# Kernel optimization log

Measured on AMD Instinct MI355X. Metric: run time of the kernel, lower is better.

Reference implementation:

```python
import jax, jax.numpy as jnp
import numpy as np

B, T, D, K = 8, 1024, 512, 1024
PRECISION = 0.1


def setup_inputs() -> dict:
    key = jax.random.key(0)
    kx, kc = jax.random.split(key)
    x = jax.random.normal(kx, (B, T, D), dtype=jnp.float32)
    codebook = jax.random.normal(kc, (K, D), dtype=jnp.float32)
    precision = PRECISION * jnp.ones((1,), dtype=jnp.float32)
    return {"x": x, "codebook": codebook, "precision": precision}


def reference(x, codebook, precision):
    # score[b,t,k] = -sum_d (x[b,t,d] - codebook[k,d])^2
    x_sq = jnp.sum(x * x, axis=-1, keepdims=True)            # [B,T,1]
    c_sq = jnp.sum(codebook * codebook, axis=-1)              # [K]
    xc = jnp.einsum('btd,kd->btk', x, codebook)               # [B,T,K] GEMM
    score = -(x_sq - 2.0 * xc + c_sq)                         # [B,T,K]
    return precision * score
```

## Files before the change

### kernel.cpp

```cpp
#include <hip/hip_runtime.h>

typedef unsigned short u16;
typedef __attribute__((ext_vector_type(8))) short short8;
typedef __attribute__((ext_vector_type(4))) float f32x4;

typedef void gvoid_t __attribute__((address_space(1)));
typedef void lvoid_t __attribute__((address_space(3)));

#define M_DIM 8192
#define N_DIM 1024
#define K_DIM 512

__device__ __forceinline__ void async_copy16(const void* g, void* l) {
  __builtin_amdgcn_global_load_lds((gvoid_t*)g, (lvoid_t*)l, 16, 0, 0);
}

__device__ __forceinline__ unsigned bf16bits(float v) {
  union { float f; unsigned u; } c; c.f = v;
  return (c.u + 0x7FFFu + ((c.u >> 16) & 1u)) >> 16;
}

__global__ __launch_bounds__(256) void cvt_sq_kernel(
    const float* __restrict__ x, const float* __restrict__ cb,
    u16* __restrict__ xb, u16* __restrict__ cbb,
    float* __restrict__ xsq, float* __restrict__ csq) {
  int row = blockIdx.x * 4 + (threadIdx.x >> 6);
  int lane = threadIdx.x & 63;
  const float* src; u16* dst; float* sq;
  if (row < M_DIM) {
    src = x + (size_t)row * K_DIM; dst = xb + (size_t)row * K_DIM; sq = xsq + row;
  } else {
    int r = row - M_DIM;
    src = cb + (size_t)r * K_DIM; dst = cbb + (size_t)r * K_DIM; sq = csq + r;
  }
  const float4* s4 = (const float4*)src;
  float4 v0 = s4[lane];
  float4 v1 = s4[lane + 64];
  float s = v0.x * v0.x + v0.y * v0.y + v0.z * v0.z + v0.w * v0.w +
            v1.x * v1.x + v1.y * v1.y + v1.z * v1.z + v1.w * v1.w;
  uint2* d2 = (uint2*)dst;
  d2[lane]      = make_uint2(bf16bits(v0.x) | (bf16bits(v0.y) << 16),
                             bf16bits(v0.z) | (bf16bits(v0.w) << 16));
  d2[lane + 64] = make_uint2(bf16bits(v1.x) | (bf16bits(v1.y) << 16),
                             bf16bits(v1.z) | (bf16bits(v1.w) << 16));
#pragma unroll
  for (int off = 32; off > 0; off >>= 1) s += __shfl_xor(s, off, 64);
  if (lane == 0) *sq = s;
}

__global__ __launch_bounds__(256) void qgemm_kernel(
    const u16* __restrict__ A, const u16* __restrict__ B,
    const float* __restrict__ xsq, const float* __restrict__ csq,
    const float* __restrict__ prec, float* __restrict__ out) {
  __shared__ char lds[65536];
  const int tid = threadIdx.x;
  const int wave = tid >> 6, lane = tid & 63;

  const int lin = blockIdx.x;
  const int xcd = lin & 7;
  const int idx = lin >> 3;
  const int ytile = (xcd << 3) | (idx & 7);
  const int xtile = idx >> 3;
  const int m0 = ytile * 128, n0 = xtile * 128;

  const int wm = wave >> 1, wn = wave & 1;
  const int srow = lane >> 3;
  const int scol = ((lane & 7) ^ srow) * 8;
  const int ml = lane & 15, q = lane >> 4;

  auto stage = [&](int k0, int buf) {
    char* base = lds + buf * 32768;
#pragma unroll
    for (int c = wave; c < 16; c += 4) {
      const u16* ga = A + (size_t)(m0 + c * 8 + srow) * K_DIM + (k0 + scol);
      async_copy16(ga, base + c * 1024);
      const u16* gb = B + (size_t)(n0 + c * 8 + srow) * K_DIM + (k0 + scol);
      async_copy16(gb, base + 16384 + c * 1024);
    }
  };

  stage(0, 0);

  const float p = prec[0];
  float csv[4];
#pragma unroll
  for (int j = 0; j < 4; j++) csv[j] = csq[n0 + wn * 64 + j * 16 + ml];

  f32x4 acc[4][4] = {};
  __syncthreads();

  for (int step = 0; step < 8; step++) {
    if (step < 7) stage((step + 1) * 64, (step + 1) & 1);
    const char* base = lds + (step & 1) * 32768;
#pragma unroll
    for (int kk = 0; kk < 2; kk++) {
      const int pcol = ((((kk << 2) | q) ^ (lane & 7)) << 4);
      short8 a[4], b[4];
#pragma unroll
      for (int i = 0; i < 4; i++) {
        a[i] = *(const short8*)(base + (wm * 64 + i * 16 + ml) * 128 + pcol);
        b[i] = *(const short8*)(base + 16384 + (wn * 64 + i * 16 + ml) * 128 + pcol);
      }
#pragma unroll
      for (int i = 0; i < 4; i++)
#pragma unroll
        for (int j = 0; j < 4; j++)
          acc[i][j] = __builtin_amdgcn_mfma_f32_16x16x32_bf16(a[i], b[j], acc[i][j], 0, 0, 0);
    }
    __syncthreads();
  }

#pragma unroll
  for (int i = 0; i < 4; i++) {
#pragma unroll
    for (int r = 0; r < 4; r++) {
      int row = m0 + wm * 64 + i * 16 + q * 4 + r;
      float xs = xsq[row];
      float* orow = out + (size_t)row * N_DIM + n0 + wn * 64 + ml;
#pragma unroll
      for (int j = 0; j < 4; j++)
        __builtin_nontemporal_store(p * (2.0f * acc[i][j][r] - xs - csv[j]),
                                    orow + j * 16);
    }
  }
}

extern "C" void kernel_launch(void* const* d_in, const int* in_sizes, int n_in,
                              void* d_out, int out_size, void* d_ws, size_t ws_size,
                              hipStream_t stream) {
  const float* x    = (const float*)d_in[0];
  const float* cb   = (const float*)d_in[1];
  const float* prec = (const float*)d_in[2];
  float* out = (float*)d_out;

  char* ws = (char*)d_ws;
  u16*   xb  = (u16*)(ws);
  u16*   cbb = (u16*)(ws + 8388608);
  float* xsq = (float*)(ws + 9437184);
  float* csq = (float*)(ws + 9469952);

  cvt_sq_kernel<<<2304, 256, 0, stream>>>(x, cb, xb, cbb, xsq, csq);
  qgemm_kernel<<<512, 256, 0, stream>>>(xb, cbb, xsq, csq, prec, out);
}
```

Before: 90.92 us.

## Fuse x bf16 conversion and squared-norm into GEMM A-tile staging

Removes the separate pass that converted x to bf16 and computed row norms. The GEMM now loads fp32 x tiles into registers, accumulates the squared norms, converts to bf16 and writes swizzled LDS, prefetching one step ahead. Only the codebook is still preconverted. This cuts a full read/write pass over x, but doubles the A-side bytes read inside the GEMM and replaces async LDS copies with register round-trips and redundant norm work across N tiles.

Result: slower. 94.16 us (+3.6%).

```diff
diff --git a/kernel.cpp b/kernel.cpp
--- a/kernel.cpp
+++ b/kernel.cpp
@@ -20,19 +20,12 @@
   return (c.u + 0x7FFFu + ((c.u >> 16) & 1u)) >> 16;
 }
 
-__global__ __launch_bounds__(256) void cvt_sq_kernel(
-    const float* __restrict__ x, const float* __restrict__ cb,
-    u16* __restrict__ xb, u16* __restrict__ cbb,
-    float* __restrict__ xsq, float* __restrict__ csq) {
+__global__ __launch_bounds__(256) void cvt_cb_kernel(
+    const float* __restrict__ cb, u16* __restrict__ cbb, float* __restrict__ csq) {
   int row = blockIdx.x * 4 + (threadIdx.x >> 6);
   int lane = threadIdx.x & 63;
-  const float* src; u16* dst; float* sq;
-  if (row < M_DIM) {
-    src = x + (size_t)row * K_DIM; dst = xb + (size_t)row * K_DIM; sq = xsq + row;
-  } else {
-    int r = row - M_DIM;
-    src = cb + (size_t)r * K_DIM; dst = cbb + (size_t)r * K_DIM; sq = csq + r;
-  }
+  const float* src = cb + (size_t)row * K_DIM;
+  u16* dst = cbb + (size_t)row * K_DIM;
   const float4* s4 = (const float4*)src;
   float4 v0 = s4[lane];
   float4 v1 = s4[lane + 64];
@@ -45,14 +38,15 @@
                              bf16bits(v1.z) | (bf16bits(v1.w) << 16));
 #pragma unroll
   for (int off = 32; off > 0; off >>= 1) s += __shfl_xor(s, off, 64);
-  if (lane == 0) *sq = s;
+  if (lane == 0) csq[row] = s;
 }
 
-__global__ __launch_bounds__(256) void qgemm_kernel(
-    const u16* __restrict__ A, const u16* __restrict__ B,
-    const float* __restrict__ xsq, const float* __restrict__ csq,
-    const float* __restrict__ prec, float* __restrict__ out) {
+__global__ __launch_bounds__(256) void qgemm_fused(
+    const float* __restrict__ X, const u16* __restrict__ Bm,
+    const float* __restrict__ csq, const float* __restrict__ prec,
+    float* __restrict__ out) {
   __shared__ char lds[65536];
+  __shared__ float xsq_lds[128];
   const int tid = threadIdx.x;
   const int wave = tid >> 6, lane = tid & 63;
 
@@ -64,33 +58,60 @@
   const int m0 = ytile * 128, n0 = xtile * 128;
 
   const int wm = wave >> 1, wn = wave & 1;
+  const int ml = lane & 15, q = lane >> 4;
   const int srow = lane >> 3;
   const int scol = ((lane & 7) ^ srow) * 8;
-  const int ml = lane & 15, q = lane >> 4;
+  const int ar = lane >> 3;
+  const int ak = lane & 7;
+  const int apos = (ak ^ ar) * 16;
 
-  auto stage = [&](int k0, int buf) {
+  float xsq_acc[4] = {0.f, 0.f, 0.f, 0.f};
+  float4 av[8];
+
+  auto loadA = [&](int k0) {
+#pragma unroll
+    for (int c = 0; c < 4; c++) {
+      const float* g = X + (size_t)(m0 + c * 32 + wave * 8 + ar) * K_DIM + k0 + ak * 8;
+      av[2 * c]     = ((const float4*)g)[0];
+      av[2 * c + 1] = ((const float4*)g)[1];
+    }
+  };
+  auto writeA = [&](int buf) {
     char* base = lds + buf * 32768;
 #pragma unroll
+    for (int c = 0; c < 4; c++) {
+      float4 v0 = av[2 * c], v1 = av[2 * c + 1];
+      xsq_acc[c] += v0.x * v0.x + v0.y * v0.y + v0.z * v0.z + v0.w * v0.w +
+                    v1.x * v1.x + v1.y * v1.y + v1.z * v1.z + v1.w * v1.w;
+      uint4 pk = make_uint4(bf16bits(v0.x) | (bf16bits(v0.y) << 16),
+                            bf16bits(v0.z) | (bf16bits(v0.w) << 16),
+                            bf16bits(v1.x) | (bf16bits(v1.y) << 16),
+                            bf16bits(v1.z) | (bf16bits(v1.w) << 16));
+      *(uint4*)(base + (c * 32 + wave * 8 + ar) * 128 + apos) = pk;
+    }
+  };
+  auto stageB = [&](int k0, int buf) {
+    char* base = lds + buf * 32768 + 16384;
+#pragma unroll
     for (int c = wave; c < 16; c += 4) {
-      const u16* ga = A + (size_t)(m0 + c * 8 + srow) * K_DIM + (k0 + scol);
-      async_copy16(ga, base + c * 1024);
-      const u16* gb = B + (size_t)(n0 + c * 8 + srow) * K_DIM + (k0 + scol);
-      async_copy16(gb, base + 16384 + c * 1024);
+      const u16* gb = Bm + (size_t)(n0 + c * 8 + srow) * K_DIM + (k0 + scol);
+      async_copy16(gb, base + c * 1024);
     }
   };
 
-  stage(0, 0);
-
+  loadA(0);
+  stageB(0, 0);
   const float p = prec[0];
   float csv[4];
 #pragma unroll
   for (int j = 0; j < 4; j++) csv[j] = csq[n0 + wn * 64 + j * 16 + ml];
+  writeA(0);
 
   f32x4 acc[4][4] = {};
   __syncthreads();
 
   for (int step = 0; step < 8; step++) {
-    if (step < 7) stage((step + 1) * 64, (step + 1) & 1);
+    if (step < 7) { loadA((step + 1) * 64); stageB((step + 1) * 64, (step + 1) & 1); }
     const char* base = lds + (step & 1) * 32768;
 #pragma unroll
     for (int kk = 0; kk < 2; kk++) {
@@ -107,16 +128,27 @@
         for (int j = 0; j < 4; j++)
           acc[i][j] = __builtin_amdgcn_mfma_f32_16x16x32_bf16(a[i], b[j], acc[i][j], 0, 0, 0);
     }
+    if (step < 7) writeA((step + 1) & 1);
     __syncthreads();
   }
+
+#pragma unroll
+  for (int c = 0; c < 4; c++) {
+    float s = xsq_acc[c];
+    s += __shfl_xor(s, 1, 64);
+    s += __shfl_xor(s, 2, 64);
+    s += __shfl_xor(s, 4, 64);
+    if (ak == 0) xsq_lds[c * 32 + wave * 8 + ar] = s;
+  }
+  __syncthreads();
 
 #pragma unroll
   for (int i = 0; i < 4; i++) {
 #pragma unroll
     for (int r = 0; r < 4; r++) {
-      int row = m0 + wm * 64 + i * 16 + q * 4 + r;
-      float xs = xsq[row];
-      float* orow = out + (size_t)row * N_DIM + n0 + wn * 64 + ml;
+      int lrow = wm * 64 + i * 16 + q * 4 + r;
+      float xs = xsq_lds[lrow];
+      float* orow = out + (size_t)(m0 + lrow) * N_DIM + n0 + wn * 64 + ml;
 #pragma unroll
       for (int j = 0; j < 4; j++)
         __builtin_nontemporal_store(p * (2.0f * acc[i][j][r] - xs - csv[j]),
@@ -134,11 +166,9 @@
   float* out = (float*)d_out;
 
   char* ws = (char*)d_ws;
-  u16*   xb  = (u16*)(ws);
-  u16*   cbb = (u16*)(ws + 8388608);
-  float* xsq = (float*)(ws + 9437184);
-  float* csq = (float*)(ws + 9469952);
+  u16*   cbb = (u16*)(ws);
+  float* csq = (float*)(ws + 1048576);
 
-  cvt_sq_kernel<<<2304, 256, 0, stream>>>(x, cb, xb, cbb, xsq, csq);
-  qgemm_kernel<<<512, 256, 0, stream>>>(xb, cbb, xsq, csq, prec, out);
+  cvt_cb_kernel<<<256, 256, 0, stream>>>(cb, cbb, csq);
+  qgemm_fused<<<512, 256, 0, stream>>>(x, cbb, csq, prec, out);
 }
```
